# Kernel tuning notes

Measured on AMD Instinct MI355X. Metric: run time of the kernel, lower is better.

## Reference

```python
import jax, jax.numpy as jnp
import numpy as np
from jax import lax

BS = 256

def layer_norm(x, w, b, eps=1e-5):
    mu = jnp.mean(x, axis=-1, keepdims=True)
    var = jnp.mean((x - mu) ** 2, axis=-1, keepdims=True)
    return (x - mu) / jnp.sqrt(var + eps) * w + b

def conv2d(x, w, b):
    y = lax.conv_general_dilated(x, w, (1, 1), 'VALID', dimension_numbers=('NCHW', 'OIHW', 'NCHW'))
    return y + b[None, :, None, None]

def max_pool2(x):
    return lax.reduce_window(x, -jnp.inf, lax.max, (1, 1, 2, 2), (1, 1, 2, 2), 'VALID')

def mha(x, wqkv, bqkv, wo, bo, nheads):
    # x: (L, B, E); torch nn.MultiheadAttention in eval mode (dropout off)
    L, B, E = x.shape
    hd = E // nheads
    qkv = jnp.einsum('lbd,ed->lbe', x, wqkv) + bqkv
    q, k, v = jnp.split(qkv, 3, axis=-1)
    q = q.reshape(L, B, nheads, hd) * (hd ** -0.5)
    k = k.reshape(L, B, nheads, hd)
    v = v.reshape(L, B, nheads, hd)
    att = jax.nn.softmax(jnp.einsum('qbhd,kbhd->bhqk', q, k), axis=-1)
    o = jnp.einsum('bhqk,kbhd->qbhd', att, v).reshape(L, B, E)
    return jnp.einsum('lbe,oe->lbo', o, wo) + bo

def grouped_mha(u, wqkv, bqkv, wo, bo, nheads):
    # u: (G, L, B, E) -- the 16 distinct small MHA blocks batched into one grouped attention
    G, L, B, E = u.shape
    hd = E // nheads
    qkv = jnp.einsum('glbd,ged->glbe', u, wqkv) + bqkv[:, None, None, :]
    q, k, v = jnp.split(qkv, 3, axis=-1)
    q = q.reshape(G, L, B, nheads, hd) * (hd ** -0.5)
    k = k.reshape(G, L, B, nheads, hd)
    v = v.reshape(G, L, B, nheads, hd)
    att = jax.nn.softmax(jnp.einsum('gqbhd,gkbhd->gbhqk', q, k), axis=-1)
    o = jnp.einsum('gbhqk,gkbhd->gqbhd', att, v).reshape(G, L, B, E)
    return jnp.einsum('glbe,goe->glbo', o, wo) + bo[:, None, None, :]

def setup_inputs() -> dict:
    key = jax.random.key(0)
    ks = iter(jax.random.split(key, 40))
    n = lambda shape, s=0.02: jax.random.normal(next(ks), shape, dtype=jnp.float32) * s
    inp = {
        't': jax.random.uniform(next(ks), (BS, 128, 128), dtype=jnp.float32) * 255.0,
        'conv1_w': n((32, 1, 3, 3), 0.1), 'conv1_b': n((32,)),
        'conv2_w': n((32, 32, 3, 3), 0.05), 'conv2_b': n((32,)),
        'expand_w': n((64, 36), 0.05), 'expand_b': n((64,)),
        'mha_wqkv': n((16, 192, 64)), 'mha_bqkv': n((16, 192)),
        'mha_wo': n((16, 64, 64)), 'mha_bo': n((16, 64)),
        'ln1_w': jnp.ones((64,), jnp.float32), 'ln1_b': jnp.zeros((64,), jnp.float32),
        'enc_wqkv': n((3 * 2048, 2048)), 'enc_bqkv': n((3 * 2048,)),
        'enc_wo': n((2048, 2048)), 'enc_bo': n((2048,)),
        'enc_ln1_w': jnp.ones((2048,), jnp.float32), 'enc_ln1_b': jnp.zeros((2048,), jnp.float32),
        'enc_w1': n((2048, 2048)), 'enc_b1': n((2048,)),
        'enc_w2': n((2048, 2048)), 'enc_b2': n((2048,)),
        'enc_ln2_w': jnp.ones((2048,), jnp.float32), 'enc_ln2_b': jnp.zeros((2048,), jnp.float32),
        'f1_w': n((512, 16 * 2048), 0.01), 'f1_b': n((512,)),
        'f2_w': n((128, 512)), 'f2_b': n((128,)),
        'f3_w': n((25, 128)), 'f3_b': n((25,)),
    }
    return inp

def reference(t, conv1_w, conv1_b, conv2_w, conv2_b, expand_w, expand_b,
              mha_wqkv, mha_bqkv, mha_wo, mha_bo, ln1_w, ln1_b,
              enc_wqkv, enc_bqkv, enc_wo, enc_bo, enc_ln1_w, enc_ln1_b,
              enc_w1, enc_b1, enc_w2, enc_b2, enc_ln2_w, enc_ln2_b,
              f1_w, f1_b, f2_w, f2_b, f3_w, f3_b):
    bs = t.shape[0]
    t = t / 255.0
    # 4x4 grid of 32x32 tiles -> (bs*16, 1, 32, 32); replaces the double python loop
    x = t.reshape(bs, 4, 32, 4, 32).transpose(0, 1, 3, 2, 4).reshape(bs * 16, 1, 32, 32)
    u = max_pool2(conv2d(x, conv1_w, conv1_b))   # (bs*16, 32, 15, 15)
    u = max_pool2(conv2d(u, conv2_w, conv2_b))   # (bs*16, 32, 6, 6)
    u = u.reshape(bs * 16, 32, 36)
    u = jax.nn.relu(u @ expand_w.T + expand_b)
    u = u.reshape(16, 32, bs, 64)                 # raw reshape, exactly as in source
    att = grouped_mha(u, mha_wqkv, mha_bqkv, mha_wo, mha_bo, 4)
    u = layer_norm(u + att, ln1_w, ln1_b)         # dropout is identity in eval
    x = u.reshape(16, bs, 2048)
    # TransformerEncoderLayer d_model=2048, nhead=16, post-norm, ReLU FFN (eval)
    a = mha(x, enc_wqkv, enc_bqkv, enc_wo, enc_bo, 16)
    x = layer_norm(x + a, enc_ln1_w, enc_ln1_b)
    ff = jax.nn.relu(x @ enc_w1.T + enc_b1) @ enc_w2.T + enc_b2
    x = layer_norm(x + ff, enc_ln2_w, enc_ln2_b)
    u = x.reshape(bs, 16 * 2048)                  # raw reshape, exactly as in source
    u = jax.nn.relu(u @ f1_w.T + f1_b)
    u = jax.nn.relu(u @ f2_w.T + f2_b)
    return u @ f3_w.T + f3_b
```

## Files before the change

kernel.cpp:

```cpp
#include <hip/hip_runtime.h>


#define EPS 1e-5f

typedef __attribute__((ext_vector_type(8))) short s16x8;
typedef __attribute__((ext_vector_type(4))) float f32x4;

__device__ inline float bf2f(ushort u) {
    union { unsigned u; float f; } x; x.u = ((unsigned)u) << 16; return x.f;
}
__device__ inline ushort f2bf(float f) {
    union { float f; unsigned u; } x; x.f = f;
    unsigned r = x.u + 0x7FFFu + ((x.u >> 16) & 1u);
    return (ushort)(r >> 16);
}
__device__ inline void gload_lds16(const void* g, void* l) {
    __builtin_amdgcn_global_load_lds(
        (const __attribute__((address_space(1))) unsigned int*)g,
        (__attribute__((address_space(3))) unsigned int*)l, 16, 0, 0);
}

__global__ __launch_bounds__(256) void conv1_pool(
    const float* __restrict__ t, const float* __restrict__ w,
    const float* __restrict__ bias, float* __restrict__ out)
{
    __shared__ float tile[32][33];
    __shared__ float ws9[288];
    __shared__ float bs[32];
    int n = blockIdx.x, tid = threadIdx.x;
    int b = n >> 4, tt = n & 15, ty = tt >> 2, tx = tt & 3;
    const float* tb = t + (long)b * 16384 + ty * 32 * 128 + tx * 32;
    for (int i = tid; i < 1024; i += 256) {
        int r = i >> 5, cc = i & 31;
        tile[r][cc] = tb[r * 128 + cc] * (1.0f / 255.0f);
    }
    for (int i = tid; i < 288; i += 256) ws9[i] = w[i];
    if (tid < 32) bs[tid] = bias[tid];
    __syncthreads();
    for (int o = tid; o < 7200; o += 256) {
        int c = o / 225, p = o - c * 225;
        int py = p / 15, px = p - py * 15;
        float in[4][4];
        #pragma unroll
        for (int iy = 0; iy < 4; ++iy) {
            #pragma unroll
            for (int ix = 0; ix < 4; ++ix) in[iy][ix] = tile[py * 2 + iy][px * 2 + ix];
        }
        float b0 = bs[c];
        float a00 = b0, a01 = b0, a10 = b0, a11 = b0;
        const float* wc = &ws9[c * 9];
        #pragma unroll
        for (int ky = 0; ky < 3; ++ky) {
            #pragma unroll
            for (int kx = 0; kx < 3; ++kx) {
                float wv = wc[ky * 3 + kx];
                a00 += in[ky][kx] * wv;     a01 += in[ky][kx + 1] * wv;
                a10 += in[ky + 1][kx] * wv; a11 += in[ky + 1][kx + 1] * wv;
            }
        }
        out[(long)n * 7200 + o] = fmaxf(fmaxf(a00, a01), fmaxf(a10, a11));
    }
}

__global__ __launch_bounds__(256) void convw_prep(
    const float* __restrict__ w, ushort* __restrict__ wk)
{
    int i = blockIdx.x * 256 + threadIdx.x;
    if (i >= 9216) return;
    int kz = i >> 10, rem = i & 1023;
    int oc = rem >> 5, ci = rem & 31;
    wk[i] = f2bf(w[oc * 288 + ci * 9 + kz]);
}

__global__ __launch_bounds__(256) void conv2_mfma(
    const float* __restrict__ u1, const ushort* __restrict__ wk,
    const float* __restrict__ bias, float* __restrict__ u2)
{
    __shared__ __align__(16) ushort tiles[2][7680];
    __shared__ float hp[2][2376];
    int tid = threadIdx.x;
    int wave = tid >> 6, lane = tid & 63;
    int n0 = blockIdx.x * 2;

    for (int u = tid; u < 1800; u += 256) {
        int img = u / 900, v = u - img * 900;
        int ks = v / 225, pos = v - ks * 225;
        int y = pos / 15, x = pos - y * 15;
        const float* src = u1 + (long)(n0 + img) * 7200 + (ks * 8) * 225 + pos;
        union { s16x8 v8; ushort us[8]; } pk;
        #pragma unroll
        for (int j = 0; j < 8; ++j) pk.us[j] = f2bf(src[j * 225]);
        int r = y * 16 + x;
        int chunk = ks ^ ((r >> 1) & 3);
        *(s16x8*)((char*)&tiles[img][0] + r * 64 + (chunk << 4)) = pk.v8;
    }
    __syncthreads();

    int img = wave >> 1, nf = wave & 1;
    int fr = lane & 15, ks4 = lane >> 4;
    int rb[9];
    #pragma unroll
    for (int m = 0; m < 9; ++m) {
        int pos = m * 16 + fr;
        int py = pos / 12, px = pos - py * 12;
        rb[m] = py * 16 + px;
    }
    f32x4 acc[9];
    #pragma unroll
    for (int m = 0; m < 9; ++m) acc[m] = (f32x4){0.f, 0.f, 0.f, 0.f};
    const char* tbase = (const char*)&tiles[img][0];
    #pragma unroll
    for (int kz = 0; kz < 9; ++kz) {
        int ky = kz / 3, kx = kz - ky * 3;
        s16x8 bf = *(const s16x8*)(wk + kz * 1024 + (nf * 16 + fr) * 32 + ks4 * 8);
        #pragma unroll
        for (int m = 0; m < 9; ++m) {
            int r = rb[m] + ky * 16 + kx;
            s16x8 af = *(const s16x8*)(tbase + r * 64 + ((ks4 ^ ((r >> 1) & 3)) << 4));
            acc[m] = __builtin_amdgcn_mfma_f32_16x16x32_bf16(af, bf, acc[m], 0, 0, 0);
        }
    }

    int oc = nf * 16 + fr;
    int cr4 = ks4 * 4;
    #pragma unroll
    for (int m = 0; m < 9; ++m) {
        float v01 = fmaxf(acc[m][0], acc[m][1]);
        float v23 = fmaxf(acc[m][2], acc[m][3]);
        int p0 = m * 16 + cr4;
        int py = p0 / 12, px0 = p0 - py * 12;
        int rowb = py * 6 + (px0 >> 1);
        hp[img][rowb * 33 + oc] = v01;
        hp[img][(rowb + 1) * 33 + oc] = v23;
    }
    __syncthreads();

    for (int u = tid; u < 2304; u += 256) {
        int im = u / 1152, v = u - im * 1152;
        int o = v / 36, opos = v - o * 36;
        int i = opos / 6, jj = opos - i * 6;
        float a = hp[im][((2 * i) * 6 + jj) * 33 + o];
        float b = hp[im][((2 * i + 1) * 6 + jj) * 33 + o];
        u2[(long)(n0 + im) * 1152 + o * 36 + opos] = fmaxf(a, b) + bias[o];
    }
}

__global__ __launch_bounds__(256) void expand_k(
    const float* __restrict__ u2, const float* __restrict__ w,
    const float* __restrict__ bias, float* __restrict__ out)
{
    __shared__ float ws[2304];
    __shared__ float xs[2304];
    __shared__ float bs[64];
    int tid = threadIdx.x;
    long r0 = (long)blockIdx.x * 64;
    const float* src = u2 + r0 * 36;
    for (int i = tid; i < 2304; i += 256) { ws[i] = w[i]; xs[i] = src[i]; }
    if (tid < 64) bs[tid] = bias[tid];
    __syncthreads();
    int row = tid >> 2, qq = tid & 3;
    float x[36];
    #pragma unroll
    for (int k4 = 0; k4 < 36; k4 += 4) *(float4*)&x[k4] = *(const float4*)&xs[row * 36 + k4];
    float res[16];
    #pragma unroll
    for (int eo = 0; eo < 16; ++eo) {
        int e = qq * 16 + eo;
        const float* wr = &ws[e * 36];
        float acc = bs[e];
        #pragma unroll
        for (int k4 = 0; k4 < 36; k4 += 4) {
            float4 wv = *(const float4*)&wr[k4];
            acc += x[k4] * wv.x + x[k4 + 1] * wv.y + x[k4 + 2] * wv.z + x[k4 + 3] * wv.w;
        }
        res[eo] = fmaxf(acc, 0.0f);
    }
    float* orow = out + (r0 + row) * 64 + qq * 16;
    #pragma unroll
    for (int v4 = 0; v4 < 4; ++v4) *(float4*)(orow + v4 * 4) = *(float4*)&res[v4 * 4];
}

template <int BM, int BN, int BK, int TM, int TN, int ACT, int SPLITK>
__global__ __launch_bounds__(256) void gemm_tn(
    const float* __restrict__ A, const float* __restrict__ B,
    const float* __restrict__ bias, float* __restrict__ C,
    int M, int N, int K, int lda, int ldb, int ldc,
    long sA, long sB, long sBias, long sC)
{
    constexpr int NTX = BN / TN;
    constexpr int KG = BK / 4;
    __shared__ float As[BK][BM + 4];
    __shared__ float Bs[BK][BN + 4];
    int tid = threadIdx.x;
    int tx = tid % NTX, ty = tid / NTX;
    int n0 = blockIdx.x * BN, m0 = blockIdx.y * BM;
    int bz = blockIdx.z;
    int batch = bz / SPLITK, kz = bz - batch * SPLITK;
    int Kc = K / SPLITK;
    int k0 = kz * Kc, k1 = k0 + Kc;
    A += (long)batch * sA; B += (long)batch * sB; C += (long)batch * sC;
    const float* bp = bias ? bias + (long)batch * sBias : nullptr;
    float acc[TM][TN] = {};
    for (int kt = k0; kt < k1; kt += BK) {
        constexpr int A4 = BM * BK / 4;
        #pragma unroll
        for (int e0 = 0; e0 < A4; e0 += 256) {
            int e = e0 + tid;
            int rr = e / KG, kg = (e - rr * KG) * 4;
            int gm = m0 + rr;
            float4 v = make_float4(0.f, 0.f, 0.f, 0.f);
            if (gm < M) v = *(const float4*)(A + (long)gm * lda + kt + kg);
            As[kg + 0][rr] = v.x; As[kg + 1][rr] = v.y; As[kg + 2][rr] = v.z; As[kg + 3][rr] = v.w;
        }
        constexpr int B4 = BN * BK / 4;
        #pragma unroll
        for (int e0 = 0; e0 < B4; e0 += 256) {
            int e = e0 + tid;
            int rr = e / KG, kg = (e - rr * KG) * 4;
            int gn = n0 + rr;
            float4 v = make_float4(0.f, 0.f, 0.f, 0.f);
            if (gn < N) v = *(const float4*)(B + (long)gn * ldb + kt + kg);
            Bs[kg + 0][rr] = v.x; Bs[kg + 1][rr] = v.y; Bs[kg + 2][rr] = v.z; Bs[kg + 3][rr] = v.w;
        }
        __syncthreads();
        #pragma unroll
        for (int k = 0; k < BK; ++k) {
            float a[TM], b[TN];
            #pragma unroll
            for (int i = 0; i < TM; i += 4) *(float4*)&a[i] = *(const float4*)&As[k][ty * TM + i];
            #pragma unroll
            for (int j = 0; j < TN; j += 4) *(float4*)&b[j] = *(const float4*)&Bs[k][tx * TN + j];
            #pragma unroll
            for (int i = 0; i < TM; ++i) {
                #pragma unroll
                for (int j = 0; j < TN; ++j) acc[i][j] += a[i] * b[j];
            }
        }
        __syncthreads();
    }
    #pragma unroll
    for (int i = 0; i < TM; ++i) {
        int gm = m0 + ty * TM + i;
        if (gm < M) {
            #pragma unroll
            for (int j = 0; j < TN; ++j) {
                int gn = n0 + tx * TN + j;
                if (gn < N) {
                    float v = acc[i][j];
                    if (SPLITK > 1) {
                        atomicAdd(&C[(long)gm * ldc + gn], v);
                    } else {
                        if (bp) v += bp[gn];
                        if (ACT == 1) v = fmaxf(v, 0.0f);
                        C[(long)gm * ldc + gn] = v;
                    }
                }
            }
        }
    }
}

template <int ACT, int OUT_MODE>
__global__ __launch_bounds__(256) void gemm_bf16(
    const ushort* __restrict__ A, const ushort* __restrict__ B,
    const float* __restrict__ bias, float* __restrict__ Cf,
    ushort* __restrict__ Cb, int M, int N, int K)
{
    __shared__ __align__(16) ushort As[8192];
    __shared__ __align__(16) ushort Bs[8192];
    int tid = threadIdx.x;
    int wave = tid >> 6, lane = tid & 63;
    int m0 = blockIdx.y * 128, n0 = blockIdx.x * 128;
    const ushort* ga = A + (long)(m0 + wave * 32 + (lane >> 3)) * K + (lane & 7) * 8;
    const ushort* gb = B + (long)(n0 + wave * 32 + (lane >> 3)) * K + (lane & 7) * 8;
    ushort* la = &As[wave * 2048];
    ushort* lb = &Bs[wave * 2048];
    int wr = wave >> 1, wc = wave & 1;
    int fr = lane & 15, ks = (lane >> 4) * 8;
    f32x4 acc[4][4];
    #pragma unroll
    for (int i = 0; i < 4; ++i)
        #pragma unroll
        for (int j = 0; j < 4; ++j) acc[i][j] = (f32x4){0.f, 0.f, 0.f, 0.f};

    for (int kt = 0; kt < K; kt += 64) {
        #pragma unroll
        for (int i = 0; i < 4; ++i) {
            gload_lds16(ga + kt + (long)i * 8 * K, la + i * 512);
            gload_lds16(gb + kt + (long)i * 8 * K, lb + i * 512);
        }
        __syncthreads();
        #pragma unroll
        for (int kk = 0; kk < 64; kk += 32) {
            s16x8 af[4], bfr[4];
            #pragma unroll
            for (int m = 0; m < 4; ++m)
                af[m] = *(const s16x8*)&As[(wr * 64 + m * 16 + fr) * 64 + kk + ks];
            #pragma unroll
            for (int n = 0; n < 4; ++n)
                bfr[n] = *(const s16x8*)&Bs[(wc * 64 + n * 16 + fr) * 64 + kk + ks];
            #pragma unroll
            for (int m = 0; m < 4; ++m)
                #pragma unroll
                for (int n = 0; n < 4; ++n)
                    acc[m][n] = __builtin_amdgcn_mfma_f32_16x16x32_bf16(
                        af[m], bfr[n], acc[m][n], 0, 0, 0);
        }
        __syncthreads();
    }
    int cr = (lane >> 4) * 4;
    #pragma unroll
    for (int n = 0; n < 4; ++n) {
        int col = n0 + wc * 64 + n * 16 + fr;
        float bv = bias ? bias[col] : 0.f;
        #pragma unroll
        for (int m = 0; m < 4; ++m) {
            #pragma unroll
            for (int j = 0; j < 4; ++j) {
                int row = m0 + wr * 64 + m * 16 + cr + j;
                float v = acc[m][n][j] + bv;
                if (ACT == 1) v = fmaxf(v, 0.f);
                if (OUT_MODE != 2) Cf[(long)row * N + col] = v;
                if (OUT_MODE != 0) Cb[(long)row * N + col] = f2bf(v);
            }
        }
    }
}

__global__ __launch_bounds__(256) void f2b_kernel(
    const float* __restrict__ in, ushort* __restrict__ out, int n8)
{
    int i = blockIdx.x * 256 + threadIdx.x;
    if (i >= n8) return;
    long base = (long)i * 8;
    float4 v0 = *(const float4*)(in + base);
    float4 v1 = *(const float4*)(in + base + 4);
    ushort4 a, b;
    a.x = f2bf(v0.x); a.y = f2bf(v0.y); a.z = f2bf(v0.z); a.w = f2bf(v0.w);
    b.x = f2bf(v1.x); b.y = f2bf(v1.y); b.z = f2bf(v1.z); b.w = f2bf(v1.w);
    *(ushort4*)(out + base) = a;
    *(ushort4*)(out + base + 4) = b;
}

__global__ __launch_bounds__(256) void gatt_ln(
    const float* __restrict__ qkv, const float* __restrict__ u,
    const float* __restrict__ wo, const float* __restrict__ bo,
    const float* __restrict__ lnw, const float* __restrict__ lnb,
    ushort* __restrict__ out)
{
    __shared__ float sm[12928];
    float* qs  = sm;
    float* ks  = sm + 2112;
    float* vs  = sm + 4160;
    float* wos = sm + 6208;
    float* os  = sm + 10560;
    float* psT = sm;
    float* bos = sm + 12736;
    float* lws = sm + 12800;
    float* lbs = sm + 12864;
    int gb = blockIdx.x;
    int g = gb >> 8, b = gb & 255;
    int tid = threadIdx.x;

    const float* base = qkv + (long)g * 1572864 + b * 192;
    for (int e = tid; e < 1536; e += 256) {
        int s = e / 48, c4 = (e - s * 48) * 4;
        float4 v = *(const float4*)(base + (long)s * 49152 + c4);
        if (c4 < 64) {
            float* q = &qs[s * 66 + c4];
            q[0] = v.x * 0.25f; q[1] = v.y * 0.25f; q[2] = v.z * 0.25f; q[3] = v.w * 0.25f;
        } else if (c4 < 128) {
            *(float4*)&ks[s * 64 + (c4 - 64)] = v;
        } else {
            *(float4*)&vs[s * 64 + (c4 - 128)] = v;
        }
    }
    const float* wog = wo + g * 4096;
    for (int i = tid; i < 4096; i += 256) wos[(i >> 6) * 68 + (i & 63)] = wog[i];
    if (tid < 64) { bos[tid] = bo[g * 64 + tid]; lws[tid] = lnw[tid]; lbs[tid] = lnb[tid]; }
    __syncthreads();

    int hr = tid >> 1;
    int h = hr >> 5, qi = hr & 31, half = tid & 1;
    float qreg[16];
    #pragma unroll
    for (int d2 = 0; d2 < 16; d2 += 2)
        *(float2*)&qreg[d2] = *(const float2*)&qs[qi * 66 + h * 16 + d2];
    float sc[16];
    #pragma unroll
    for (int jj = 0; jj < 16; ++jj) {
        int j = half * 16 + jj;
        const float* kr = &ks[j * 64 + h * 16];
        float a = 0.f;
        #pragma unroll
        for (int d4 = 0; d4 < 16; d4 += 4) {
            float4 kv = *(const float4*)&kr[d4];
            a += qreg[d4] * kv.x + qreg[d4 + 1] * kv.y + qreg[d4 + 2] * kv.z + qreg[d4 + 3] * kv.w;
        }
        sc[jj] = a;
    }
    float mx = sc[0];
    #pragma unroll
    for (int jj = 1; jj < 16; ++jj) mx = fmaxf(mx, sc[jj]);
    mx = fmaxf(mx, __shfl_xor(mx, 1));
    float sum = 0.f;
    #pragma unroll
    for (int jj = 0; jj < 16; ++jj) { sc[jj] = __expf(sc[jj] - mx); sum += sc[jj]; }
    sum += __shfl_xor(sum, 1);
    float inv = 1.0f / sum;
    __syncthreads();
    #pragma unroll
    for (int jj = 0; jj < 16; ++jj)
        psT[(half * 16 + jj) * 128 + h * 32 + qi] = sc[jj] * inv;
    __syncthreads();

    int si = tid >> 3, e0 = (tid & 7) * 8;
    int hh = e0 >> 4;
    float oacc[8] = {};
    for (int j = 0; j < 32; ++j) {
        float pj = psT[j * 128 + hh * 32 + si];
        const float* vr = &vs[j * 64 + e0];
        float4 v0 = *(const float4*)&vr[0];
        float4 v1 = *(const float4*)&vr[4];
        oacc[0] += pj * v0.x; oacc[1] += pj * v0.y; oacc[2] += pj * v0.z; oacc[3] += pj * v0.w;
        oacc[4] += pj * v1.x; oacc[5] += pj * v1.y; oacc[6] += pj * v1.z; oacc[7] += pj * v1.w;
    }
    #pragma unroll
    for (int e = 0; e < 8; ++e) os[si * 68 + e0 + e] = oacc[e];
    __syncthreads();

    int r8 = tid & 7;
    float z[8];
    {
        float accq[8];
        #pragma unroll
        for (int q = 0; q < 8; ++q) accq[q] = bos[r8 + q * 8];
        #pragma unroll 4
        for (int e4 = 0; e4 < 64; e4 += 4) {
            float4 ov = *(const float4*)&os[si * 68 + e4];
            #pragma unroll
            for (int q = 0; q < 8; ++q) {
                float4 wv = *(const float4*)&wos[(r8 + q * 8) * 68 + e4];
                accq[q] += ov.x * wv.x + ov.y * wv.y + ov.z * wv.z + ov.w * wv.w;
            }
        }
        long ubase = (((long)g * 32 + si) * 256 + b) * 64;
        #pragma unroll
        for (int q = 0; q < 8; ++q) z[q] = accq[q] + u[ubase + r8 + q * 8];
    }
    float s1 = 0.f, s2 = 0.f;
    #pragma unroll
    for (int q = 0; q < 8; ++q) { s1 += z[q]; s2 += z[q] * z[q]; }
    #pragma unroll
    for (int off = 1; off < 8; off <<= 1) { s1 += __shfl_xor(s1, off); s2 += __shfl_xor(s2, off); }
    float mu = s1 * 0.015625f;
    float var = s2 * 0.015625f - mu * mu;
    float rstd = rsqrtf(var + EPS);
    long obase = (((long)g * 32 + si) * 256 + b) * 64;
    #pragma unroll
    for (int q = 0; q < 8; ++q) {
        int e2 = r8 + q * 8;
        out[obase + e2] = f2bf((z[q] - mu) * rstd * lws[e2] + lbs[e2]);
    }
}

__global__ __launch_bounds__(256) void enc_att(
    const float* __restrict__ qkv, ushort* __restrict__ o)
{
    __shared__ float qs[16 * 132], ks[16 * 132], vs[16 * 132], ps[16 * 17];
    int bh = blockIdx.x;
    int b2 = bh >> 4, h = bh & 15;
    int tid = threadIdx.x;
    const float qscale = 0.08838834764831845f;
    for (int e = tid; e < 512; e += 256) {
        int l = e >> 5, c4 = (e & 31) * 4;
        long rowoff = ((long)l * 256 + b2) * 6144 + h * 128 + c4;
        float4 q = *(const float4*)(qkv + rowoff);
        float4 k = *(const float4*)(qkv + rowoff + 2048);
        float4 v = *(const float4*)(qkv + rowoff + 4096);
        q.x *= qscale; q.y *= qscale; q.z *= qscale; q.w *= qscale;
        *(float4*)&qs[l * 132 + c4] = q;
        *(float4*)&ks[l * 132 + c4] = k;
        *(float4*)&vs[l * 132 + c4] = v;
    }
    __syncthreads();
    int qi = tid >> 4, j = tid & 15;
    float acc = 0.f;
    #pragma unroll
    for (int d = 0; d < 128; d += 4) {
        float4 qv = *(const float4*)&qs[qi * 132 + d];
        float4 kv = *(const float4*)&ks[j * 132 + d];
        acc += qv.x * kv.x + qv.y * kv.y + qv.z * kv.z + qv.w * kv.w;
    }
    float m = acc;
    #pragma unroll
    for (int off = 1; off < 16; off <<= 1) m = fmaxf(m, __shfl_xor(m, off));
    float p = __expf(acc - m);
    float sum = p;
    #pragma unroll
    for (int off = 1; off < 16; off <<= 1) sum += __shfl_xor(sum, off);
    ps[qi * 17 + j] = p / sum;
    __syncthreads();
    float pr[16];
    #pragma unroll
    for (int jj = 0; jj < 16; ++jj) pr[jj] = ps[qi * 17 + jj];
    long obase = ((long)qi * 256 + b2) * 2048 + h * 128;
    #pragma unroll
    for (int qd = 0; qd < 8; ++qd) {
        int d = (tid & 15) + qd * 16;
        float a = 0.f;
        #pragma unroll
        for (int jj = 0; jj < 16; ++jj) a += pr[jj] * vs[jj * 132 + d];
        o[obase + d] = f2bf(a);
    }
}

template <int RSD_BF, int OUT_BF>
__global__ __launch_bounds__(256) void resid_ln(
    const float* __restrict__ y, const void* __restrict__ rsdv,
    const float* __restrict__ w, const float* __restrict__ bb,
    float* __restrict__ out, ushort* __restrict__ outb)
{
    __shared__ float red[8];
    int tid = threadIdx.x;
    long row = blockIdx.x;
    const float* yr = y + row * 2048;
    float4 a0 = *(const float4*)(yr + tid * 4);
    float4 a1 = *(const float4*)(yr + 1024 + tid * 4);
    float r[8];
    if (RSD_BF) {
        const ushort* rr = (const ushort*)rsdv + row * 2048;
        ushort4 u0 = *(const ushort4*)(rr + tid * 4);
        ushort4 u1 = *(const ushort4*)(rr + 1024 + tid * 4);
        r[0] = bf2f(u0.x); r[1] = bf2f(u0.y); r[2] = bf2f(u0.z); r[3] = bf2f(u0.w);
        r[4] = bf2f(u1.x); r[5] = bf2f(u1.y); r[6] = bf2f(u1.z); r[7] = bf2f(u1.w);
    } else {
        const float* rr = (const float*)rsdv + row * 2048;
        float4 r0 = *(const float4*)(rr + tid * 4);
        float4 r1 = *(const float4*)(rr + 1024 + tid * 4);
        r[0] = r0.x; r[1] = r0.y; r[2] = r0.z; r[3] = r0.w;
        r[4] = r1.x; r[5] = r1.y; r[6] = r1.z; r[7] = r1.w;
    }
    float v[8] = { a0.x + r[0], a0.y + r[1], a0.z + r[2], a0.w + r[3],
                   a1.x + r[4], a1.y + r[5], a1.z + r[6], a1.w + r[7] };
    float s1 = 0.f, s2 = 0.f;
    #pragma unroll
    for (int i = 0; i < 8; ++i) { s1 += v[i]; s2 += v[i] * v[i]; }
    #pragma unroll
    for (int off = 1; off < 64; off <<= 1) { s1 += __shfl_xor(s1, off); s2 += __shfl_xor(s2, off); }
    int wid = tid >> 6, lane = tid & 63;
    if (lane == 0) { red[wid * 2] = s1; red[wid * 2 + 1] = s2; }
    __syncthreads();
    s1 = red[0] + red[2] + red[4] + red[6];
    s2 = red[1] + red[3] + red[5] + red[7];
    float mu = s1 * (1.0f / 2048.0f);
    float var = s2 * (1.0f / 2048.0f) - mu * mu;
    float rstd = rsqrtf(var + EPS);
    float4 w0 = *(const float4*)(w + tid * 4);
    float4 w1 = *(const float4*)(w + 1024 + tid * 4);
    float4 b0 = *(const float4*)(bb + tid * 4);
    float4 b1 = *(const float4*)(bb + 1024 + tid * 4);
    float o0[8];
    o0[0] = (v[0] - mu) * rstd * w0.x + b0.x; o0[1] = (v[1] - mu) * rstd * w0.y + b0.y;
    o0[2] = (v[2] - mu) * rstd * w0.z + b0.z; o0[3] = (v[3] - mu) * rstd * w0.w + b0.w;
    o0[4] = (v[4] - mu) * rstd * w1.x + b1.x; o0[5] = (v[5] - mu) * rstd * w1.y + b1.y;
    o0[6] = (v[6] - mu) * rstd * w1.z + b1.z; o0[7] = (v[7] - mu) * rstd * w1.w + b1.w;
    *(float4*)(out + row * 2048 + tid * 4) = *(float4*)&o0[0];
    *(float4*)(out + row * 2048 + 1024 + tid * 4) = *(float4*)&o0[4];
    if (OUT_BF) {
        ushort4 q0, q1;
        q0.x = f2bf(o0[0]); q0.y = f2bf(o0[1]); q0.z = f2bf(o0[2]); q0.w = f2bf(o0[3]);
        q1.x = f2bf(o0[4]); q1.y = f2bf(o0[5]); q1.z = f2bf(o0[6]); q1.w = f2bf(o0[7]);
        *(ushort4*)(outb + row * 2048 + tid * 4) = q0;
        *(ushort4*)(outb + row * 2048 + 1024 + tid * 4) = q1;
    }
}

__global__ __launch_bounds__(256) void bias_relu_f1(
    float* __restrict__ x, const float* __restrict__ b)
{
    int i = blockIdx.x * 256 + threadIdx.x;
    float v = x[i] + b[i & 511];
    x[i] = fmaxf(v, 0.0f);
}

extern "C" void kernel_launch(void* const* d_in, const int* in_sizes, int n_in,
                              void* d_out, int out_size, void* d_ws, size_t ws_size,
                              hipStream_t stream)
{
    (void)in_sizes; (void)n_in; (void)out_size; (void)ws_size;
    const float* t        = (const float*)d_in[0];
    const float* conv1_w  = (const float*)d_in[1];
    const float* conv1_b  = (const float*)d_in[2];
    const float* conv2_w  = (const float*)d_in[3];
    const float* conv2_b  = (const float*)d_in[4];
    const float* expand_w = (const float*)d_in[5];
    const float* expand_b = (const float*)d_in[6];
    const float* mha_wqkv = (const float*)d_in[7];
    const float* mha_bqkv = (const float*)d_in[8];
    const float* mha_wo   = (const float*)d_in[9];
    const float* mha_bo   = (const float*)d_in[10];
    const float* ln1_w    = (const float*)d_in[11];
    const float* ln1_b    = (const float*)d_in[12];
    const float* enc_wqkv = (const float*)d_in[13];
    const float* enc_bqkv = (const float*)d_in[14];
    const float* enc_wo   = (const float*)d_in[15];
    const float* enc_bo   = (const float*)d_in[16];
    const float* enc_ln1w = (const float*)d_in[17];
    const float* enc_ln1b = (const float*)d_in[18];
    const float* enc_w1   = (const float*)d_in[19];
    const float* enc_b1   = (const float*)d_in[20];
    const float* enc_w2   = (const float*)d_in[21];
    const float* enc_b2   = (const float*)d_in[22];
    const float* enc_ln2w = (const float*)d_in[23];
    const float* enc_ln2b = (const float*)d_in[24];
    const float* f1_w     = (const float*)d_in[25];
    const float* f1_b     = (const float*)d_in[26];
    const float* f2_w     = (const float*)d_in[27];
    const float* f2_b     = (const float*)d_in[28];
    const float* f3_w     = (const float*)d_in[29];
    const float* f3_b     = (const float*)d_in[30];
    float* out = (float*)d_out;

    float* W = (float*)d_ws;
    float*  u1     = W;
    float*  u2     = W + 29491200;
    float*  u      = W + 34209792;
    float*  qkvg   = W;
    ushort* uln_b  = (ushort*)(W + 42598400);
    ushort* wk     = (ushort*)(W + 46800000);
    ushort* wqkv_b = (ushort*)(W);
    ushort* wo_b   = (ushort*)(W + 6291456);
    ushort* w1_b   = (ushort*)(W + 33554432);
    ushort* w2_b   = (ushort*)(W + 35651584);
    float*  qkv2   = W + 8388608;
    ushort* obuf_b = (ushort*)(W + 37748736);
    float*  ytmp   = W + 8388608;
    float*  x1     = W + 16777216;
    ushort* x1_b   = (ushort*)(W + 25165824);
    ushort* hbuf_b = (ushort*)(W + 29360128);
    float*  x2     = W;
    float*  f1o    = W + 8388608;
    float*  f2o    = W + 8519680;

    dim3 blk(256);
    convw_prep<<<36, blk, 0, stream>>>(conv2_w, wk);
    conv1_pool<<<4096, blk, 0, stream>>>(t, conv1_w, conv1_b, u1);
    conv2_mfma<<<2048, blk, 0, stream>>>(u1, wk, conv2_b, u2);
    expand_k<<<2048, blk, 0, stream>>>(u2, expand_w, expand_b, u);
    gemm_tn<64, 64, 16, 4, 4, 0, 1><<<dim3(3, 128, 16), blk, 0, stream>>>(
        u, mha_wqkv, mha_bqkv, qkvg, 8192, 192, 64, 64, 64, 192,
        524288L, 12288L, 192L, 1572864L);
    gatt_ln<<<4096, blk, 0, stream>>>(qkvg, u, mha_wo, mha_bo, ln1_w, ln1_b, uln_b);
    f2b_kernel<<<6144, blk, 0, stream>>>(enc_wqkv, wqkv_b, 1572864);
    f2b_kernel<<<2048, blk, 0, stream>>>(enc_wo, wo_b, 524288);
    f2b_kernel<<<2048, blk, 0, stream>>>(enc_w1, w1_b, 524288);
    f2b_kernel<<<2048, blk, 0, stream>>>(enc_w2, w2_b, 524288);
    gemm_bf16<0, 0><<<dim3(48, 32), blk, 0, stream>>>(
        uln_b, wqkv_b, enc_bqkv, qkv2, nullptr, 4096, 6144, 2048);
    enc_att<<<4096, blk, 0, stream>>>(qkv2, obuf_b);
    gemm_bf16<0, 0><<<dim3(16, 32), blk, 0, stream>>>(
        obuf_b, wo_b, enc_bo, ytmp, nullptr, 4096, 2048, 2048);
    resid_ln<1, 1><<<4096, blk, 0, stream>>>(ytmp, uln_b, enc_ln1w, enc_ln1b, x1, x1_b);
    gemm_bf16<1, 2><<<dim3(16, 32), blk, 0, stream>>>(
        x1_b, w1_b, enc_b1, nullptr, hbuf_b, 4096, 2048, 2048);
    gemm_bf16<0, 0><<<dim3(16, 32), blk, 0, stream>>>(
        hbuf_b, w2_b, enc_b2, ytmp, nullptr, 4096, 2048, 2048);
    resid_ln<0, 0><<<4096, blk, 0, stream>>>(ytmp, x1, enc_ln2w, enc_ln2b, x2, nullptr);
    hipMemsetAsync(f1o, 0, 131072 * sizeof(float), stream);
    gemm_tn<64, 64, 16, 4, 4, 0, 64><<<dim3(8, 4, 64), blk, 0, stream>>>(
        x2, f1_w, nullptr, f1o, 256, 512, 32768, 32768, 32768, 512, 0, 0, 0, 0);
    bias_relu_f1<<<512, blk, 0, stream>>>(f1o, f1_b);
    gemm_tn<64, 64, 16, 4, 4, 1, 1><<<dim3(2, 4, 1), blk, 0, stream>>>(
        f1o, f2_w, f2_b, f2o, 256, 128, 512, 512, 512, 128, 0, 0, 0, 0);
    gemm_tn<64, 64, 16, 4, 4, 0, 1><<<dim3(1, 4, 1), blk, 0, stream>>>(
        f2o, f3_w, f3_b, out, 256, 25, 128, 128, 128, 25, 0, 0, 0, 0);
}
```

Baseline: 1.164 ms.

## Store conv1 output as bf16 and run f1 as split-K bf16 MFMA GEMM

```diff
diff --git a/kernel.cpp b/kernel.cpp
--- a/kernel.cpp
+++ b/kernel.cpp
@@ -22,7 +22,7 @@
 
 __global__ __launch_bounds__(256) void conv1_pool(
     const float* __restrict__ t, const float* __restrict__ w,
-    const float* __restrict__ bias, float* __restrict__ out)
+    const float* __restrict__ bias, ushort* __restrict__ out)
 {
     __shared__ float tile[32][33];
     __shared__ float ws9[288];
@@ -58,7 +58,7 @@
                 a10 += in[ky + 1][kx] * wv; a11 += in[ky + 1][kx + 1] * wv;
             }
         }
-        out[(long)n * 7200 + o] = fmaxf(fmaxf(a00, a01), fmaxf(a10, a11));
+        out[(long)n * 7200 + o] = f2bf(fmaxf(fmaxf(a00, a01), fmaxf(a10, a11)));
     }
 }
 
@@ -73,7 +73,7 @@
 }
 
 __global__ __launch_bounds__(256) void conv2_mfma(
-    const float* __restrict__ u1, const ushort* __restrict__ wk,
+    const ushort* __restrict__ u1, const ushort* __restrict__ wk,
     const float* __restrict__ bias, float* __restrict__ u2)
 {
     __shared__ __align__(16) ushort tiles[2][7680];
@@ -86,10 +86,10 @@
         int img = u / 900, v = u - img * 900;
         int ks = v / 225, pos = v - ks * 225;
         int y = pos / 15, x = pos - y * 15;
-        const float* src = u1 + (long)(n0 + img) * 7200 + (ks * 8) * 225 + pos;
+        const ushort* src = u1 + (long)(n0 + img) * 7200 + (ks * 8) * 225 + pos;
         union { s16x8 v8; ushort us[8]; } pk;
         #pragma unroll
-        for (int j = 0; j < 8; ++j) pk.us[j] = f2bf(src[j * 225]);
+        for (int j = 0; j < 8; ++j) pk.us[j] = src[j * 225];
         int r = y * 16 + x;
         int chunk = ks ^ ((r >> 1) & 3);
         *(s16x8*)((char*)&tiles[img][0] + r * 64 + (chunk << 4)) = pk.v8;
@@ -260,7 +260,7 @@
     }
 }
 
-template <int ACT, int OUT_MODE>
+template <int ACT, int OUT_MODE, int SPLITK = 1>
 __global__ __launch_bounds__(256) void gemm_bf16(
     const ushort* __restrict__ A, const ushort* __restrict__ B,
     const float* __restrict__ bias, float* __restrict__ Cf,
@@ -283,7 +283,9 @@
         #pragma unroll
         for (int j = 0; j < 4; ++j) acc[i][j] = (f32x4){0.f, 0.f, 0.f, 0.f};
 
-    for (int kt = 0; kt < K; kt += 64) {
+    int k0 = 0, k1 = K;
+    if (SPLITK > 1) { int Kc = K / SPLITK; k0 = blockIdx.z * Kc; k1 = k0 + Kc; }
+    for (int kt = k0; kt < k1; kt += 64) {
         #pragma unroll
         for (int i = 0; i < 4; ++i) {
             gload_lds16(ga + kt + (long)i * 8 * K, la + i * 512);
@@ -312,19 +314,34 @@
     #pragma unroll
     for (int n = 0; n < 4; ++n) {
         int col = n0 + wc * 64 + n * 16 + fr;
-        float bv = bias ? bias[col] : 0.f;
+        float bv = (SPLITK == 1 && bias) ? bias[col] : 0.f;
         #pragma unroll
         for (int m = 0; m < 4; ++m) {
             #pragma unroll
             for (int j = 0; j < 4; ++j) {
                 int row = m0 + wr * 64 + m * 16 + cr + j;
                 float v = acc[m][n][j] + bv;
-                if (ACT == 1) v = fmaxf(v, 0.f);
-                if (OUT_MODE != 2) Cf[(long)row * N + col] = v;
-                if (OUT_MODE != 0) Cb[(long)row * N + col] = f2bf(v);
+                if (SPLITK > 1) {
+                    Cf[(long)blockIdx.z * M * N + (long)row * N + col] = v;
+                } else {
+                    if (ACT == 1) v = fmaxf(v, 0.f);
+                    if (OUT_MODE != 2) Cf[(long)row * N + col] = v;
+                    if (OUT_MODE != 0) Cb[(long)row * N + col] = f2bf(v);
+                }
             }
         }
     }
+}
+
+__global__ __launch_bounds__(256) void f1_reduce(
+    const float* __restrict__ part, const float* __restrict__ bias,
+    float* __restrict__ out)
+{
+    int i = blockIdx.x * 256 + threadIdx.x;
+    float s = 0.f;
+    #pragma unroll 8
+    for (int k = 0; k < 64; ++k) s += part[(long)k * 131072 + i];
+    out[i] = fmaxf(s + bias[i & 511], 0.f);
 }
 
 __global__ __launch_bounds__(256) void f2b_kernel(
@@ -574,14 +591,6 @@
         *(ushort4*)(outb + row * 2048 + tid * 4) = q0;
         *(ushort4*)(outb + row * 2048 + 1024 + tid * 4) = q1;
     }
-}
-
-__global__ __launch_bounds__(256) void bias_relu_f1(
-    float* __restrict__ x, const float* __restrict__ b)
-{
-    int i = blockIdx.x * 256 + threadIdx.x;
-    float v = x[i] + b[i & 511];
-    x[i] = fmaxf(v, 0.0f);
 }
 
 extern "C" void kernel_launch(void* const* d_in, const int* in_sizes, int n_in,
@@ -623,7 +632,7 @@
     float* out = (float*)d_out;
 
     float* W = (float*)d_ws;
-    float*  u1     = W;
+    ushort* u1b    = (ushort*)W;
     float*  u2     = W + 29491200;
     float*  u      = W + 34209792;
     float*  qkvg   = W;
@@ -640,13 +649,16 @@
     ushort* x1_b   = (ushort*)(W + 25165824);
     ushort* hbuf_b = (ushort*)(W + 29360128);
     float*  x2     = W;
-    float*  f1o    = W + 8388608;
-    float*  f2o    = W + 8519680;
+    ushort* x2_b   = (ushort*)(W + 37748736);
+    ushort* f1w_b  = (ushort*)(W + 25165824);
+    float*  f1part = W + 8388608;
+    float*  f1o    = W + 16777216;
+    float*  f2o    = W + 16908288;
 
     dim3 blk(256);
     convw_prep<<<36, blk, 0, stream>>>(conv2_w, wk);
-    conv1_pool<<<4096, blk, 0, stream>>>(t, conv1_w, conv1_b, u1);
-    conv2_mfma<<<2048, blk, 0, stream>>>(u1, wk, conv2_b, u2);
+    conv1_pool<<<4096, blk, 0, stream>>>(t, conv1_w, conv1_b, u1b);
+    conv2_mfma<<<2048, blk, 0, stream>>>(u1b, wk, conv2_b, u2);
     expand_k<<<2048, blk, 0, stream>>>(u2, expand_w, expand_b, u);
     gemm_tn<64, 64, 16, 4, 4, 0, 1><<<dim3(3, 128, 16), blk, 0, stream>>>(
         u, mha_wqkv, mha_bqkv, qkvg, 8192, 192, 64, 64, 64, 192,
@@ -666,11 +678,11 @@
         x1_b, w1_b, enc_b1, nullptr, hbuf_b, 4096, 2048, 2048);
     gemm_bf16<0, 0><<<dim3(16, 32), blk, 0, stream>>>(
         hbuf_b, w2_b, enc_b2, ytmp, nullptr, 4096, 2048, 2048);
-    resid_ln<0, 0><<<4096, blk, 0, stream>>>(ytmp, x1, enc_ln2w, enc_ln2b, x2, nullptr);
-    hipMemsetAsync(f1o, 0, 131072 * sizeof(float), stream);
-    gemm_tn<64, 64, 16, 4, 4, 0, 64><<<dim3(8, 4, 64), blk, 0, stream>>>(
-        x2, f1_w, nullptr, f1o, 256, 512, 32768, 32768, 32768, 512, 0, 0, 0, 0);
-    bias_relu_f1<<<512, blk, 0, stream>>>(f1o, f1_b);
+    resid_ln<0, 1><<<4096, blk, 0, stream>>>(ytmp, x1, enc_ln2w, enc_ln2b, x2, x2_b);
+    f2b_kernel<<<8192, blk, 0, stream>>>(f1_w, f1w_b, 2097152);
+    gemm_bf16<0, 0, 64><<<dim3(4, 2, 64), blk, 0, stream>>>(
+        x2_b, f1w_b, nullptr, f1part, nullptr, 256, 512, 32768);
+    f1_reduce<<<512, blk, 0, stream>>>(f1part, f1_b, f1o);
     gemm_tn<64, 64, 16, 4, 4, 1, 1><<<dim3(2, 4, 1), blk, 0, stream>>>(
         f1o, f2_w, f2_b, f2o, 256, 128, 512, 512, 512, 128, 0, 0, 0, 0);
     gemm_tn<64, 64, 16, 4, 4, 0, 1><<<dim3(1, 4, 1), blk, 0, stream>>>(
```

Measured after the change: 1.005 ms. 13.7% less time.
